# Performance work log

Hardware: AMD Instinct MI355X
Metric: run time of the kernel (lower is better)

Reference implementation:

```python
import jax, jax.numpy as jnp
import numpy as np

B, N, C, K = 2, 8192, 128, 16

def _mlp2(h, W1, b1, W2, b2):
    return jax.nn.relu(h @ W1 + b1) @ W2 + b2

def setup_inputs() -> dict:
    key = jax.random.key(0)
    ks = jax.random.split(key, 20)
    s = lambda d: 1.0 / np.sqrt(d)
    inp = {
        "x": jax.random.normal(ks[0], (B, N, C), jnp.float32),
        "position": jax.random.normal(ks[1], (B, N, 3), jnp.float32),
        "Wq": jax.random.normal(ks[2], (C, C), jnp.float32) * s(C),
        "bq": jnp.zeros((C,), jnp.float32),
        "Wk": jax.random.normal(ks[3], (C, C), jnp.float32) * s(C),
        "bk": jnp.zeros((C,), jnp.float32),
        "Wv": jax.random.normal(ks[4], (C, C), jnp.float32) * s(C),
        "bv": jnp.zeros((C,), jnp.float32),
        "Wp1": jax.random.normal(ks[5], (3, C), jnp.float32) * s(3),
        "bp1": jnp.zeros((C,), jnp.float32),
        "Wp2": jax.random.normal(ks[6], (C, C), jnp.float32) * s(C),
        "bp2": jnp.zeros((C,), jnp.float32),
        "Wg1": jax.random.normal(ks[7], (C, C), jnp.float32) * s(C),
        "bg1": jnp.zeros((C,), jnp.float32),
        "Wg2": jax.random.normal(ks[8], (C, C), jnp.float32) * s(C),
        "bg2": jnp.zeros((C,), jnp.float32),
    }
    return inp

def reference(x, position, Wq, bq, Wk, bk, Wv, bv, Wp1, bp1, Wp2, bp2, Wg1, bg1, Wg2, bg2):
    # kNN via squared pairwise distances (monotone in cdist, same topk indices)
    p2 = jnp.sum(position * position, axis=-1)                       # (B,N)
    d2 = p2[:, :, None] + p2[:, None, :] - 2.0 * jnp.einsum("bnd,bmd->bnm", position, position)
    _, idx = jax.lax.top_k(-d2, K)                                    # (B,N,K) nearest (incl self)

    gather = jax.vmap(lambda arr, i: arr[i])                          # per-batch fancy gather
    neighbors = gather(x, idx)                                        # (B,N,K,C)
    pos_nb = gather(position, idx)                                    # (B,N,K,3)

    q = x @ Wq + bq                                                   # (B,N,C)
    k = neighbors @ Wk + bk                                           # (B,N,K,C)
    v = neighbors @ Wv + bv                                           # (B,N,K,C)

    # positional MLP only at gathered pairs (same math as all-pairs-then-gather)
    rel = position[:, :, None, :] - pos_nb                            # (B,N,K,3)
    pe = _mlp2(rel, Wp1, bp1, Wp2, bp2)                               # (B,N,K,C)

    scale = 1.0 / jnp.sqrt(jnp.float32(C))
    attn = (q[:, :, None, :] - k + pe) * scale
    attn = _mlp2(attn, Wg1, bg1, Wg2, bg2)
    attn = jax.nn.softmax(attn, axis=2)                               # softmax over K neighbors
    out = jnp.sum(attn * (v + pe), axis=2)                            # (B,N,C)
    return out
```

## Files before the change

### kernel.cpp

```cpp
#include <hip/hip_runtime.h>
#include <hip/hip_bf16.h>
#include <stdint.h>

#define NPTS 8192
#define CDIM 128
#define KNNK 16
#define WELEMF 16384
#define SCALE 0.08838834764831845f
#define FLDS_BYTES 78848
#define GRES 16
#define NCELL (GRES*GRES*GRES)

typedef __attribute__((ext_vector_type(4))) float f32x4;
typedef __attribute__((ext_vector_type(8))) short s16x8;

__device__ __forceinline__ unsigned short to_bf16(float f){
  union { __hip_bfloat16 h; unsigned short u; } v;
  v.h = __float2bfloat16(f);
  return v.u;
}

__device__ __forceinline__ s16x8 cvt8(const float* p){
  float4 lo = *(const float4*)p;
  float4 hi = *(const float4*)(p + 4);
  s16x8 f;
  f[0]=(short)to_bf16(lo.x); f[1]=(short)to_bf16(lo.y);
  f[2]=(short)to_bf16(lo.z); f[3]=(short)to_bf16(lo.w);
  f[4]=(short)to_bf16(hi.x); f[5]=(short)to_bf16(hi.y);
  f[6]=(short)to_bf16(hi.z); f[7]=(short)to_bf16(hi.w);
  return f;
}

__device__ __forceinline__ unsigned mapf_u(unsigned s){
  return s ^ (0x80000000u | (unsigned)(((int)s) >> 31));
}
__device__ __forceinline__ float unmapf_u(unsigned u){
  unsigned r = (u & 0x80000000u) ? (u ^ 0x80000000u) : ~u;
  return __uint_as_float(r);
}

__global__ __launch_bounds__(256) void zero_init_kernel(int* __restrict__ counts,
                                                        unsigned* __restrict__ bbox)
{
  int t = blockIdx.x*256 + threadIdx.x;
  if (t < 2*NCELL) counts[t] = 0;
  if (t < 12) bbox[t] = ((t % 6) < 3) ? 0xFFFFFFFFu : 0u;
}

__global__ __launch_bounds__(256) void prep_kernel(
    const float* __restrict__ Wq, const float* __restrict__ Wk,
    const float* __restrict__ Wv, const float* __restrict__ Wp2,
    const float* __restrict__ Wg1, const float* __restrict__ Wg2,
    const float* __restrict__ pos,
    unsigned short* __restrict__ wt, float4* __restrict__ pos4,
    unsigned* __restrict__ bbox)
{
  int t = blockIdx.x*256 + threadIdx.x;
  if (t < 6*WELEMF){
    int w = t >> 14, f = t & (WELEMF-1);
    int i = f & 7, ln = (f >> 3) & 63, kkct = f >> 9;
    int kk = kkct & 3, ct = kkct >> 2;
    int kdim = kk*32 + (ln >> 4)*8 + i, col = ct*16 + (ln & 15);
    const float* src = (w==0)?Wq:(w==1)?Wk:(w==2)?Wv:(w==3)?Wp2:(w==4)?Wg1:Wg2;
    float v = src[kdim*CDIM + col];
    if (w == 1) v = -v;
    wt[t] = to_bf16(v);
  } else {
    int m = t - 6*WELEMF;
    float xx = pos[m*3+0], yy = pos[m*3+1], zz = pos[m*3+2];
    float p2 = __fadd_rn(__fadd_rn(__fmul_rn(xx,xx), __fmul_rn(yy,yy)), __fmul_rn(zz,zz));
    pos4[m] = make_float4(xx, yy, zz, p2);
    unsigned mnx = mapf_u(__float_as_uint(xx)), mny = mapf_u(__float_as_uint(yy)), mnz = mapf_u(__float_as_uint(zz));
    unsigned mxx = mnx, mxy = mny, mxz = mnz;
#pragma unroll
    for (int off = 1; off < 64; off <<= 1){
      mnx = min(mnx, (unsigned)__shfl_xor((int)mnx, off));
      mny = min(mny, (unsigned)__shfl_xor((int)mny, off));
      mnz = min(mnz, (unsigned)__shfl_xor((int)mnz, off));
      mxx = max(mxx, (unsigned)__shfl_xor((int)mxx, off));
      mxy = max(mxy, (unsigned)__shfl_xor((int)mxy, off));
      mxz = max(mxz, (unsigned)__shfl_xor((int)mxz, off));
    }
    if ((threadIdx.x & 63) == 0){
      int b = m >> 13;
      atomicMin(&bbox[b*6+0], mnx); atomicMin(&bbox[b*6+1], mny); atomicMin(&bbox[b*6+2], mnz);
      atomicMax(&bbox[b*6+3], mxx); atomicMax(&bbox[b*6+4], mxy); atomicMax(&bbox[b*6+5], mxz);
    }
  }
}

__global__ __launch_bounds__(256) void bin_count_kernel(
    const float4* __restrict__ pos4, const unsigned* __restrict__ bbox,
    int* __restrict__ counts, int* __restrict__ cellId)
{
  int m = blockIdx.x*256 + threadIdx.x;
  int b = m >> 13;
  float4 p = pos4[m];
  float lox = unmapf_u(bbox[b*6+0]), loy = unmapf_u(bbox[b*6+1]), loz = unmapf_u(bbox[b*6+2]);
  float hix = unmapf_u(bbox[b*6+3]), hiy = unmapf_u(bbox[b*6+4]), hiz = unmapf_u(bbox[b*6+5]);
  int ix = min(GRES-1, max(0, (int)((p.x - lox) * ((float)GRES/(hix-lox)))));
  int iy = min(GRES-1, max(0, (int)((p.y - loy) * ((float)GRES/(hiy-loy)))));
  int iz = min(GRES-1, max(0, (int)((p.z - loz) * ((float)GRES/(hiz-loz)))));
  int cid = (iz*GRES + iy)*GRES + ix;
  cellId[m] = cid;
  atomicAdd(&counts[b*NCELL + cid], 1);
}

__global__ __launch_bounds__(1024) void scan_kernel(
    const int* __restrict__ counts, int* __restrict__ starts, int* __restrict__ cursor)
{
  __shared__ int part[1024];
  int b = blockIdx.x, t = threadIdx.x;
  const int* c = counts + b*NCELL;
  int* s = starts + b*(NCELL+1);
  int* cur = cursor + b*NCELL;
  int base = t*4, sum = 0;
  for (int i = 0; i < 4; ++i) sum += c[base+i];
  part[t] = sum; __syncthreads();
  for (int off = 1; off < 1024; off <<= 1){
    int v = (t >= off) ? part[t-off] : 0;
    __syncthreads();
    part[t] += v;
    __syncthreads();
  }
  int run = (t > 0) ? part[t-1] : 0;
  for (int i = 0; i < 4; ++i){ int cc = c[base+i]; s[base+i] = run; cur[base+i] = run; run += cc; }
  if (t == 1023) s[NCELL] = run;
}

__global__ __launch_bounds__(256) void scatter_kernel(
    const float4* __restrict__ pos4, const int* __restrict__ cellId,
    int* __restrict__ cursor, float4* __restrict__ spos4)
{
  int m = blockIdx.x*256 + threadIdx.x;
  int b = m >> 13;
  float4 p = pos4[m];
  int dst = atomicAdd(&cursor[b*NCELL + cellId[m]], 1);
  spos4[(b<<13) + dst] = make_float4(p.x, p.y, p.z, __uint_as_float((unsigned)(m & (NPTS-1))));
}

__global__ __launch_bounds__(256) void knn_grid_kernel(
    const float4* __restrict__ spos4, const int* __restrict__ starts,
    const unsigned* __restrict__ bbox, int* __restrict__ idxout)
{
  const int tid = threadIdx.x, lane = tid & 63;
  const int sub = lane >> 4, sl = lane & 15, gbase = sub*16;
  const int w = tid >> 6;
  const int g = blockIdx.x*16 + w*4 + sub;
  const int b = g >> 13, n = g & (NPTS-1);
  const float4* sp = spos4 + ((size_t)b<<13);
  const int*    st = starts + b*(NCELL+1);

  const float4 q4 = sp[n];
  const int orig = __float_as_int(q4.w);
  const float qx = q4.x, qy = q4.y, qz = q4.z;
  const float q2 = __fadd_rn(__fadd_rn(__fmul_rn(qx,qx), __fmul_rn(qy,qy)), __fmul_rn(qz,qz));

  float lox = unmapf_u(bbox[b*6+0]), loy = unmapf_u(bbox[b*6+1]), loz = unmapf_u(bbox[b*6+2]);
  float hix = unmapf_u(bbox[b*6+3]), hiy = unmapf_u(bbox[b*6+4]), hiz = unmapf_u(bbox[b*6+5]);
  float cwx = (hix-lox)*(1.0f/GRES), cwy = (hiy-loy)*(1.0f/GRES), cwz = (hiz-loz)*(1.0f/GRES);
  int cx = min(GRES-1, max(0, (int)((qx - lox) * ((float)GRES/(hix-lox)))));
  int cy = min(GRES-1, max(0, (int)((qy - loy) * ((float)GRES/(hiy-loy)))));
  int cz = min(GRES-1, max(0, (int)((qz - loz) * ((float)GRES/(hiz-loz)))));

  unsigned khi = 0xFFFFFFFFu, klo = 0xFFFFFFFFu;
  float Tf = __builtin_inff();

  auto insert = [&](unsigned ihi, unsigned ilo){
    unsigned phi = (unsigned)__builtin_amdgcn_update_dpp(0, (int)khi, 0x111, 0xF, 0xF, false);
    unsigned plo = (unsigned)__builtin_amdgcn_update_dpp(0, (int)klo, 0x111, 0xF, 0xF, false);
    bool gt  = (khi > ihi) || (khi == ihi && klo > ilo);
    bool pgt = (sl != 0) && ((phi > ihi) || (phi == ihi && plo > ilo));
    khi = gt ? (pgt ? phi : ihi) : khi;
    klo = gt ? (pgt ? plo : ilo) : klo;
  };
  auto updT = [&](){
    unsigned t15 = (unsigned)__shfl((int)khi, gbase + 15);
    Tf = (t15 >= 0xFF800000u) ? __builtin_inff() : unmapf_u(t15);
  };

  bool gdone = false;
  for (int R = 1; R <= GRES-1; ++R){
    const bool first = (R == 1);
    const int per = 8*R, w1 = 2*R-1;
    const int ntask = first ? 9 : (per + 2*w1*w1);
    for (int tb = 0; tb < ntask; tb += 16){
      int t = tb + sl;
      int dy = 0, dz = 0, gx0 = 0, gx1 = -1;
      bool valid = (!gdone) && (t < ntask);
      if (first){
        if (valid){ dy = t % 3 - 1; dz = t / 3 - 1; }
        gx0 = max(cx-1, 0); gx1 = min(cx+1, GRES-1);
      } else if (valid){
        if (t < per){
          int s2 = 2*(2*R+1);
          if (t < s2){ dz = (t < 2*R+1) ? -R : R; dy = t % (2*R+1) - R; }
          else { int u = t - s2; dy = (u & 1) ? R : -R; dz = (u >> 1) - (R-1); }
          gx0 = max(cx-R, 0); gx1 = min(cx+R, GRES-1);
        } else {
          int i = t - per, ri = i >> 1;
          dy = ri % w1 - (R-1); dz = ri / w1 - (R-1);
          int gx = cx + ((i & 1) ? R : -R);
          gx0 = gx; gx1 = gx;
          valid = gx >= 0 && gx <= GRES-1;
        }
      }
      int gy = cy + dy, gz = cz + dz;
      valid = valid && gy >= 0 && gy < GRES && gz >= 0 && gz < GRES && gx0 <= gx1;
      int s0 = 0, s1 = 0;
      if (valid){ int cb = (gz*GRES + gy)*GRES; s0 = st[cb + gx0]; s1 = st[cb + gx1 + 1]; }
      unsigned long long bal = __ballot(valid && (s1 > s0));
      unsigned cm = (unsigned)((bal >> gbase) & 0xFFFFull);
      while (__any(cm != 0)){
        bool act = (cm != 0);
        int srow = act ? __builtin_ctz(cm) : 0;
        if (act) cm &= cm - 1;
        int cs = __shfl(s0, gbase + srow);
        int ce = __shfl(s1, gbase + srow);
        if (!act){ cs = 0; ce = 0; }
        for (int p0 = cs; p0 < ce; p0 += 16){
          int mm = p0 + sl;
          bool v = mm < ce;
          float4 c = v ? sp[mm] : make_float4(0.f,0.f,0.f,0.f);
          float c2  = __fadd_rn(__fadd_rn(__fmul_rn(c.x,c.x), __fmul_rn(c.y,c.y)), __fmul_rn(c.z,c.z));
          float dot = __builtin_fmaf(c.z, qz, __builtin_fmaf(c.y, qy, __fmul_rn(c.x, qx)));
          float d2  = __fsub_rn(__fadd_rn(q2, c2), __fadd_rn(dot, dot));
          int oi = __float_as_int(c.w);
          bool ins = v && (d2 <= Tf);
          unsigned long long ib = __ballot(ins);
          unsigned im = (unsigned)((ib >> gbase) & 0xFFFFull);
          if (__any(im != 0)){
            while (__any(im != 0)){
              bool a2 = (im != 0);
              int s = a2 ? __builtin_ctz(im) : 0;
              if (a2) im &= im - 1;
              unsigned dvb = (unsigned)__shfl((int)__float_as_uint(d2), gbase + s);
              int ov = __shfl(oi, gbase + s);
              if (a2) insert(mapf_u(dvb), (unsigned)ov);
            }
            updT();
          }
        }
      }
    }
    const float big = 1e30f;
    float dxlo = (cx-R <= 0)      ? big : (qx - (lox + (float)(cx-R)*cwx));
    float dxhi = (cx+R >= GRES-1) ? big : ((lox + (float)(cx+R+1)*cwx) - qx);
    float dylo = (cy-R <= 0)      ? big : (qy - (loy + (float)(cy-R)*cwy));
    float dyhi = (cy+R >= GRES-1) ? big : ((loy + (float)(cy+R+1)*cwy) - qy);
    float dzlo = (cz-R <= 0)      ? big : (qz - (loz + (float)(cz-R)*cwz));
    float dzhi = (cz+R >= GRES-1) ? big : ((loz + (float)(cz+R+1)*cwz) - qz);
    float dmin = fminf(fminf(fminf(dxlo,dxhi), fminf(dylo,dyhi)), fminf(dzlo,dzhi));
    bool full = dmin >= 1e29f;
    dmin = fmaxf(dmin, 0.0f);
    float dmin2 = dmin*dmin;
    bool stop = full || (Tf + 1e-4f + Tf*1e-5f < dmin2);
    gdone = gdone || stop;
    if (__all(gdone)) break;
  }
  idxout[(((size_t)b<<13) + orig)*KNNK + sl] = (int)klo;
}

__global__ __launch_bounds__(512, 2) void fused_kernel(
    const float* __restrict__ x, const float* __restrict__ pos,
    const float* __restrict__ bq, const float* __restrict__ bk,
    const float* __restrict__ bv, const float* __restrict__ Wp1,
    const float* __restrict__ bp1, const float* __restrict__ bp2,
    const float* __restrict__ bg1, const float* __restrict__ bg2,
    const int* __restrict__ idxws, const unsigned short* __restrict__ wt,
    float* __restrict__ out)
{
  extern __shared__ char smem[];
  char* Sbase = smem;
  char* Tbase = smem + 32768;
  float* blds = (float*)(smem + 65536);
  float* q_lds = (float*)(smem + 70656);

  const int tid = threadIdx.x;
  const int lane = tid & 63, w = tid >> 6;
  const int r = lane & 15, grp = lane >> 4;
  const int pbase = blockIdx.x * 16;
  const int b = pbase >> 13;

  auto gll = [&](int s, char* dst){
#pragma unroll
    for (int k = 0; k < 4; ++k){
      int c = w*4 + k;
      unsigned short* g = const_cast<unsigned short*>(wt) + (size_t)s*WELEMF + c*512 + lane*8;
      __builtin_amdgcn_global_load_lds(
        (const __attribute__((address_space(1))) void*)g,
        (__attribute__((address_space(3))) void*)(dst + c*1024), 16, 0, 0);
    }
  };
  auto ldS = [&](int ct, int kk) -> s16x8 {
    return *(const s16x8*)&((unsigned short*)Sbase)[((ct*4 + kk)*64 + lane)*8];
  };
  auto ldT = [&](int ct, int kk) -> s16x8 {
    return *(const s16x8*)&((unsigned short*)Tbase)[((ct*4 + kk)*64 + lane)*8];
  };

  gll(0, Sbase);
  gll(3, Tbase);

  for (int e = tid; e < 1280; e += 512){
    float v;
    if      (e < 128)  v = bq[e];
    else if (e < 256)  v = bk[e-128];
    else if (e < 384)  v = bv[e-256];
    else if (e < 512)  v = bp2[e-384];
    else if (e < 640)  v = bg1[e-512];
    else if (e < 768)  v = bg2[e-640];
    else if (e < 896)  v = bp1[e-768];
    else               v = Wp1[e-896];
    blds[e] = v;
  }
  int nbr[2]; float relx[2], rely[2], relz[2];
#pragma unroll
  for (int j = 0; j < 2; ++j){
    int gp = pbase + w*2 + j;
    nbr[j] = idxws[(size_t)gp*KNNK + r];
    const float* pq = pos + (size_t)gp*3;
    const float* pn = pos + ((size_t)b*NPTS + nbr[j])*3;
    relx[j] = pq[0]-pn[0]; rely[j] = pq[1]-pn[1]; relz[j] = pq[2]-pn[2];
  }
  s16x8 qa[4];
  {
    const float* xr = x + (size_t)(pbase + r)*CDIM;
#pragma unroll
    for (int kk = 0; kk < 4; ++kk) qa[kk] = cvt8(xr + kk*32 + grp*8);
  }
  __syncthreads();

  {
    f32x4 qacc = (f32x4){0.f,0.f,0.f,0.f};
#pragma unroll
    for (int kk = 0; kk < 4; ++kk)
      qacc = __builtin_amdgcn_mfma_f32_16x16x32_bf16(qa[kk], ldS(w,kk), qacc, 0,0,0);
    int col = w*16 + r;
#pragma unroll
    for (int jj = 0; jj < 4; ++jj){
      int row = grp*4 + jj;
      q_lds[row*CDIM + col] = qacc[jj] + blds[col];
    }
  }
  s16x8 pf[2][4];
#pragma unroll
  for (int j = 0; j < 2; ++j)
#pragma unroll
    for (int kk = 0; kk < 4; ++kk){
      s16x8 f;
#pragma unroll
      for (int i = 0; i < 8; ++i){
        int kc = kk*32 + grp*8 + i;
        float s = relx[j]*blds[896+kc] + rely[j]*blds[1024+kc] + relz[j]*blds[1152+kc] + blds[768+kc];
        f[i] = (short)to_bf16(fmaxf(s, 0.f));
      }
      pf[j][kk] = f;
    }
  __syncthreads();
  gll(1, Sbase);

  f32x4 at[2][8], av[2][8];
#pragma unroll
  for (int j=0;j<2;++j)
#pragma unroll
    for (int ct=0;ct<8;++ct) at[j][ct] = (f32x4){0.f,0.f,0.f,0.f};
#pragma unroll
  for (int ct=0;ct<8;++ct)
#pragma unroll
    for (int kk=0;kk<4;++kk){
      s16x8 bw = ldT(ct,kk);
#pragma unroll
      for (int j=0;j<2;++j)
        at[j][ct] = __builtin_amdgcn_mfma_f32_16x16x32_bf16(pf[j][kk], bw, at[j][ct], 0,0,0);
    }
  s16x8 nf[2][4];
#pragma unroll
  for (int j=0;j<2;++j)
#pragma unroll
    for (int kk=0;kk<4;++kk)
      nf[j][kk] = cvt8(x + ((size_t)b*NPTS + nbr[j])*CDIM + kk*32 + grp*8);

  __syncthreads();
  gll(2, Tbase);
#pragma unroll
  for (int j=0;j<2;++j)
#pragma unroll
    for (int ct=0;ct<8;++ct) av[j][ct] = at[j][ct];
#pragma unroll
  for (int ct=0;ct<8;++ct)
#pragma unroll
    for (int kk=0;kk<4;++kk){
      s16x8 bw = ldS(ct,kk);
#pragma unroll
      for (int j=0;j<2;++j) at[j][ct] = __builtin_amdgcn_mfma_f32_16x16x32_bf16(nf[j][kk], bw, at[j][ct], 0,0,0);
    }
  __syncthreads();
  gll(4, Sbase);
#pragma unroll
  for (int ct=0;ct<8;++ct)
#pragma unroll
    for (int kk=0;kk<4;++kk){
      s16x8 bw = ldT(ct,kk);
#pragma unroll
      for (int j=0;j<2;++j) av[j][ct] = __builtin_amdgcn_mfma_f32_16x16x32_bf16(nf[j][kk], bw, av[j][ct], 0,0,0);
    }
#pragma unroll
  for (int j=0;j<2;++j){
    int prow = (w*2+j)*CDIM;
#pragma unroll
    for (int ct=0;ct<8;++ct){
      int col = ct*16+r;
      float add = q_lds[prow+col] + blds[384+col] - blds[128+col];
#pragma unroll
      for (int jj=0;jj<4;++jj) at[j][ct][jj] = (at[j][ct][jj] + add)*SCALE;
    }
  }
  __syncthreads();

  unsigned short* tj = (unsigned short*)Tbase + w*2048;
  s16x8 tf[2][4];
#pragma unroll
  for (int j=0;j<2;++j){
#pragma unroll
    for (int ct=0;ct<8;++ct){
      int base = (ct>>1)*512 + ((ct&1)*2 + (r>>3))*128 + (r&7);
#pragma unroll
      for (int jj=0;jj<4;++jj)
        tj[base + (grp*4+jj)*8] = to_bf16(at[j][ct][jj]);
    }
#pragma unroll
    for (int kk=0;kk<4;++kk)
      tf[j][kk] = *(const s16x8*)&tj[(kk*64 + lane)*8];
  }
  f32x4 hacc[2][8];
#pragma unroll
  for (int j=0;j<2;++j)
#pragma unroll
    for (int ct=0;ct<8;++ct) hacc[j][ct] = (f32x4){0.f,0.f,0.f,0.f};
#pragma unroll
  for (int ct=0;ct<8;++ct)
#pragma unroll
    for (int kk=0;kk<4;++kk){
      s16x8 bw = ldS(ct,kk);
#pragma unroll
      for (int j=0;j<2;++j)
        hacc[j][ct] = __builtin_amdgcn_mfma_f32_16x16x32_bf16(tf[j][kk], bw, hacc[j][ct], 0,0,0);
    }
  __syncthreads();
  gll(5, Sbase);
  s16x8 hf[2][4];
#pragma unroll
  for (int j=0;j<2;++j){
#pragma unroll
    for (int ct=0;ct<8;++ct){
      int base = (ct>>1)*512 + ((ct&1)*2 + (r>>3))*128 + (r&7);
      int col = ct*16+r; float bb = blds[512+col];
#pragma unroll
      for (int jj=0;jj<4;++jj)
        tj[base + (grp*4+jj)*8] = to_bf16(fmaxf(hacc[j][ct][jj]+bb, 0.f));
    }
#pragma unroll
    for (int kk=0;kk<4;++kk)
      hf[j][kk] = *(const s16x8*)&tj[(kk*64 + lane)*8];
  }
  __syncthreads();
  f32x4 gacc[2][8];
#pragma unroll
  for (int j=0;j<2;++j)
#pragma unroll
    for (int ct=0;ct<8;++ct) gacc[j][ct] = (f32x4){0.f,0.f,0.f,0.f};
#pragma unroll
  for (int ct=0;ct<8;++ct)
#pragma unroll
    for (int kk=0;kk<4;++kk){
      s16x8 bw = ldS(ct,kk);
#pragma unroll
      for (int j=0;j<2;++j)
        gacc[j][ct] = __builtin_amdgcn_mfma_f32_16x16x32_bf16(hf[j][kk], bw, gacc[j][ct], 0,0,0);
    }
#pragma unroll
  for (int j=0;j<2;++j){
#pragma unroll
    for (int ct=0;ct<8;++ct){
      int col = ct*16+r;
      float gb = blds[640+col];
      float g0v = gacc[j][ct][0]+gb, g1v = gacc[j][ct][1]+gb;
      float g2v = gacc[j][ct][2]+gb, g3v = gacc[j][ct][3]+gb;
      float mx = fmaxf(fmaxf(g0v,g1v), fmaxf(g2v,g3v));
      mx = fmaxf(mx, __shfl_xor(mx,16));
      mx = fmaxf(mx, __shfl_xor(mx,32));
      float e0=__expf(g0v-mx), e1=__expf(g1v-mx), e2=__expf(g2v-mx), e3=__expf(g3v-mx);
      float vb = blds[256+col] + blds[384+col];
      float ss = e0+e1+e2+e3;
      float oo = e0*(av[j][ct][0]+vb) + e1*(av[j][ct][1]+vb)
               + e2*(av[j][ct][2]+vb) + e3*(av[j][ct][3]+vb);
      ss += __shfl_xor(ss,16); ss += __shfl_xor(ss,32);
      oo += __shfl_xor(oo,16); oo += __shfl_xor(oo,32);
      if (grp == 0) out[(size_t)(pbase + w*2 + j)*CDIM + col] = oo/ss;
    }
  }
}

extern "C" void kernel_launch(void* const* d_in, const int* in_sizes, int n_in,
                              void* d_out, int out_size, void* d_ws, size_t ws_size,
                              hipStream_t stream)
{
  const float* x    = (const float*)d_in[0];
  const float* pos  = (const float*)d_in[1];
  const float* Wq   = (const float*)d_in[2];
  const float* bq   = (const float*)d_in[3];
  const float* Wk   = (const float*)d_in[4];
  const float* bk   = (const float*)d_in[5];
  const float* Wv   = (const float*)d_in[6];
  const float* bv   = (const float*)d_in[7];
  const float* Wp1  = (const float*)d_in[8];
  const float* bp1  = (const float*)d_in[9];
  const float* Wp2  = (const float*)d_in[10];
  const float* bp2  = (const float*)d_in[11];
  const float* Wg1  = (const float*)d_in[12];
  const float* bg1  = (const float*)d_in[13];
  const float* Wg2  = (const float*)d_in[14];
  const float* bg2  = (const float*)d_in[15];
  float* out = (float*)d_out;

  char* ws = (char*)d_ws;
  int*            idxs   = (int*)ws;
  unsigned short* wt     = (unsigned short*)(ws + 1048576);
  float4*         pos4   = (float4*)(ws + 1257472);
  float4*         spos4  = (float4*)(ws + 1519616);
  int*            cellId = (int*)(ws + 1847296);
  int*            counts = (int*)(ws + 1912832);
  int*            starts = (int*)(ws + 2174976);
  int*            cursor = (int*)(ws + 2437376);
  unsigned*       bbox   = (unsigned*)(ws + 2699520);

  hipFuncSetAttribute((const void*)fused_kernel,
                      hipFuncAttributeMaxDynamicSharedMemorySize, FLDS_BYTES);

  zero_init_kernel<<<32, 256, 0, stream>>>(counts, bbox);
  prep_kernel<<<448, 256, 0, stream>>>(Wq, Wk, Wv, Wp2, Wg1, Wg2, pos, wt, pos4, bbox);
  bin_count_kernel<<<64, 256, 0, stream>>>(pos4, bbox, counts, cellId);
  scan_kernel<<<2, 1024, 0, stream>>>(counts, starts, cursor);
  scatter_kernel<<<64, 256, 0, stream>>>(pos4, cellId, cursor, spos4);
  knn_grid_kernel<<<1024, 256, 0, stream>>>(spos4, starts, bbox, idxs);
  fused_kernel<<<1024, 512, FLDS_BYTES, stream>>>(x, pos, bq, bk, bv, Wp1, bp1, bp2,
                                                  bg1, bg2, idxs, wt, out);
}
```

Before: 211.2 us.

## Stage neighborhood candidate points and cell starts into LDS for kNN grid search

Each block cooperatively loads the cell-start table and the sorted candidate points for a 7x5x5 cell box around a representative query cell into shared memory, assigning per-row offsets up to a fixed capacity. The kNN candidate loop then reads from LDS when a cell row is staged and falls back to global memory otherwise. This aims to cut repeated global/L2 loads of the same candidate points across the 16 queries in a block, at the cost of about 40KB of LDS (reducing occupancy), extra syncs, and a serial prefix loop on one thread.

```diff
diff --git a/kernel.cpp b/kernel.cpp
--- a/kernel.cpp
+++ b/kernel.cpp
@@ -10,6 +10,8 @@
 #define FLDS_BYTES 78848
 #define GRES 16
 #define NCELL (GRES*GRES*GRES)
+#define KCAP 2560
+#define UNSTAGED 0x40000000
 
 typedef __attribute__((ext_vector_type(4))) float f32x4;
 typedef __attribute__((ext_vector_type(8))) short s16x8;
@@ -143,6 +145,11 @@
     const float4* __restrict__ spos4, const int* __restrict__ starts,
     const unsigned* __restrict__ bbox, int* __restrict__ idxout)
 {
+  __shared__ float4 ptsLds[KCAP];
+  __shared__ int    stLds[25*8];
+  __shared__ int    rowBase[25];
+  __shared__ int    mcell[4];
+
   const int tid = threadIdx.x, lane = tid & 63;
   const int sub = lane >> 4, sl = lane & 15, gbase = sub*16;
   const int w = tid >> 6;
@@ -162,6 +169,36 @@
   int cx = min(GRES-1, max(0, (int)((qx - lox) * ((float)GRES/(hix-lox)))));
   int cy = min(GRES-1, max(0, (int)((qy - loy) * ((float)GRES/(hiy-loy)))));
   int cz = min(GRES-1, max(0, (int)((qz - loz) * ((float)GRES/(hiz-loz)))));
+
+  if (tid == 128){ mcell[0] = cx; mcell[1] = cy; mcell[2] = cz; }
+  __syncthreads();
+  const int bx0 = max(mcell[0]-3, 0), bx1 = min(mcell[0]+3, GRES-1);
+  const int by0 = max(mcell[1]-2, 0), by1 = min(mcell[1]+2, GRES-1);
+  const int bz0 = max(mcell[2]-2, 0), bz1 = min(mcell[2]+2, GRES-1);
+  const int xe = bx1-bx0+1, ye = by1-by0+1, ze = bz1-bz0+1;
+  const int nrows = ye*ze;
+  for (int e = tid; e < nrows*(xe+1); e += 256){
+    int ri = e/(xe+1), xi = e - ri*(xe+1);
+    int gy = by0 + ri % ye, gz = bz0 + ri / ye;
+    stLds[ri*8 + xi] = st[(gz*GRES + gy)*GRES + bx0 + xi];
+  }
+  __syncthreads();
+  if (tid == 0){
+    int cum = 0;
+    for (int ri = 0; ri < nrows; ++ri){
+      int g0 = stLds[ri*8], len = stLds[ri*8+xe] - g0;
+      if (cum + len <= KCAP){ rowBase[ri] = cum - g0; cum += len; }
+      else rowBase[ri] = UNSTAGED;
+    }
+  }
+  __syncthreads();
+  for (int ri = 0; ri < nrows; ++ri){
+    int rb = rowBase[ri];
+    if (rb == UNSTAGED) continue;
+    int g0 = stLds[ri*8], g1 = stLds[ri*8+xe];
+    for (int i = g0 + tid; i < g1; i += 256) ptsLds[rb + i] = sp[i];
+  }
+  __syncthreads();
 
   unsigned khi = 0xFFFFFFFFu, klo = 0xFFFFFFFFu;
   float Tf = __builtin_inff();
@@ -207,8 +244,19 @@
       }
       int gy = cy + dy, gz = cz + dz;
       valid = valid && gy >= 0 && gy < GRES && gz >= 0 && gz < GRES && gx0 <= gx1;
-      int s0 = 0, s1 = 0;
-      if (valid){ int cb = (gz*GRES + gy)*GRES; s0 = st[cb + gx0]; s1 = st[cb + gx1 + 1]; }
+      int s0 = 0, s1 = 0, lbase = UNSTAGED;
+      if (valid){
+        bool inbox = gy >= by0 && gy <= by1 && gz >= bz0 && gz <= bz1
+                  && gx0 >= bx0 && gx1 <= bx1;
+        if (inbox){
+          int ri = (gz-bz0)*ye + (gy-by0);
+          s0 = stLds[ri*8 + (gx0-bx0)];
+          s1 = stLds[ri*8 + (gx1-bx0+1)];
+          lbase = rowBase[ri];
+        } else {
+          int cb = (gz*GRES + gy)*GRES; s0 = st[cb + gx0]; s1 = st[cb + gx1 + 1];
+        }
+      }
       unsigned long long bal = __ballot(valid && (s1 > s0));
       unsigned cm = (unsigned)((bal >> gbase) & 0xFFFFull);
       while (__any(cm != 0)){
@@ -217,11 +265,14 @@
         if (act) cm &= cm - 1;
         int cs = __shfl(s0, gbase + srow);
         int ce = __shfl(s1, gbase + srow);
+        int lb = __shfl(lbase, gbase + srow);
         if (!act){ cs = 0; ce = 0; }
         for (int p0 = cs; p0 < ce; p0 += 16){
           int mm = p0 + sl;
           bool v = mm < ce;
-          float4 c = v ? sp[mm] : make_float4(0.f,0.f,0.f,0.f);
+          float4 c;
+          if (v) c = (lb != UNSTAGED) ? ptsLds[lb + mm] : sp[mm];
+          else   c = make_float4(0.f,0.f,0.f,0.f);
           float c2  = __fadd_rn(__fadd_rn(__fmul_rn(c.x,c.x), __fmul_rn(c.y,c.y)), __fmul_rn(c.z,c.z));
           float dot = __builtin_fmaf(c.z, qz, __builtin_fmaf(c.y, qy, __fmul_rn(c.x, qx)));
           float d2  = __fsub_rn(__fadd_rn(q2, c2), __fadd_rn(dot, dot));
```

Result: slower. 248.5 us (+17.7%).

## Fuse grid-build stages into one kernel and pre-convert x to bf16

Applied to the files above, without the earlier changes.

Replaces the separate zero-init, bbox, bin-count, scan and scatter kernels with one per-batch kernel that does counting, scanning and scattering in shared memory. This removes four launches and the global atomics on counts and cursor. prep_kernel now also converts x to a bf16 copy in the workspace, so the fused kernel can load bf16 neighbor rows directly and skip converting them from fp32 on every gather. The bf16 path is used only when the workspace is large enough and falls back to the old path otherwise. The grid build now runs on just 2 blocks, which limits its parallelism.

```diff
diff --git a/kernel.cpp b/kernel.cpp
--- a/kernel.cpp
+++ b/kernel.cpp
@@ -39,24 +39,97 @@
   return __uint_as_float(r);
 }
 
-__global__ __launch_bounds__(256) void zero_init_kernel(int* __restrict__ counts,
-                                                        unsigned* __restrict__ bbox)
+__global__ __launch_bounds__(1024) void gridbuild_kernel(
+    const float* __restrict__ pos, float4* __restrict__ spos4,
+    int* __restrict__ starts, unsigned* __restrict__ bboxg)
 {
-  int t = blockIdx.x*256 + threadIdx.x;
-  if (t < 2*NCELL) counts[t] = 0;
-  if (t < 12) bbox[t] = ((t % 6) < 3) ? 0xFFFFFFFFu : 0u;
+  __shared__ int cnt[NCELL];
+  __shared__ int part[1024];
+  __shared__ unsigned bbl[6];
+  const int b = blockIdx.x, t = threadIdx.x;
+  for (int i = t; i < NCELL; i += 1024) cnt[i] = 0;
+  if (t < 3) bbl[t] = 0xFFFFFFFFu;
+  else if (t < 6) bbl[t] = 0u;
+  __syncthreads();
+
+  float4 p[8];
+  unsigned mn0=~0u, mn1=~0u, mn2=~0u, mx0=0u, mx1=0u, mx2=0u;
+#pragma unroll
+  for (int i = 0; i < 8; ++i){
+    int m = t + i*1024;
+    const float* pp = pos + ((size_t)b*NPTS + m)*3;
+    float xx = pp[0], yy = pp[1], zz = pp[2];
+    float p2 = __fadd_rn(__fadd_rn(__fmul_rn(xx,xx), __fmul_rn(yy,yy)), __fmul_rn(zz,zz));
+    p[i] = make_float4(xx, yy, zz, p2);
+    unsigned ux = mapf_u(__float_as_uint(xx));
+    unsigned uy = mapf_u(__float_as_uint(yy));
+    unsigned uz = mapf_u(__float_as_uint(zz));
+    mn0 = min(mn0, ux); mn1 = min(mn1, uy); mn2 = min(mn2, uz);
+    mx0 = max(mx0, ux); mx1 = max(mx1, uy); mx2 = max(mx2, uz);
+  }
+#pragma unroll
+  for (int off = 1; off < 64; off <<= 1){
+    mn0 = min(mn0, (unsigned)__shfl_xor((int)mn0, off));
+    mn1 = min(mn1, (unsigned)__shfl_xor((int)mn1, off));
+    mn2 = min(mn2, (unsigned)__shfl_xor((int)mn2, off));
+    mx0 = max(mx0, (unsigned)__shfl_xor((int)mx0, off));
+    mx1 = max(mx1, (unsigned)__shfl_xor((int)mx1, off));
+    mx2 = max(mx2, (unsigned)__shfl_xor((int)mx2, off));
+  }
+  if ((t & 63) == 0){
+    atomicMin(&bbl[0], mn0); atomicMin(&bbl[1], mn1); atomicMin(&bbl[2], mn2);
+    atomicMax(&bbl[3], mx0); atomicMax(&bbl[4], mx1); atomicMax(&bbl[5], mx2);
+  }
+  __syncthreads();
+  const float lox = unmapf_u(bbl[0]), loy = unmapf_u(bbl[1]), loz = unmapf_u(bbl[2]);
+  const float hix = unmapf_u(bbl[3]), hiy = unmapf_u(bbl[4]), hiz = unmapf_u(bbl[5]);
+
+  int cid[8];
+#pragma unroll
+  for (int i = 0; i < 8; ++i){
+    int ix = min(GRES-1, max(0, (int)((p[i].x - lox) * ((float)GRES/(hix-lox)))));
+    int iy = min(GRES-1, max(0, (int)((p[i].y - loy) * ((float)GRES/(hiy-loy)))));
+    int iz = min(GRES-1, max(0, (int)((p[i].z - loz) * ((float)GRES/(hiz-loz)))));
+    cid[i] = (iz*GRES + iy)*GRES + ix;
+    atomicAdd(&cnt[cid[i]], 1);
+  }
+  __syncthreads();
+  const int base = t*4;
+  int c0 = cnt[base], c1 = cnt[base+1], c2 = cnt[base+2], c3 = cnt[base+3];
+  part[t] = c0+c1+c2+c3;
+  __syncthreads();
+  for (int off = 1; off < 1024; off <<= 1){
+    int v = (t >= off) ? part[t-off] : 0;
+    __syncthreads();
+    part[t] += v;
+    __syncthreads();
+  }
+  int run = (t > 0) ? part[t-1] : 0;
+  int* stb = starts + b*(NCELL+1);
+  int r1 = run + c0, r2 = r1 + c1, r3 = r2 + c2;
+  stb[base] = run; stb[base+1] = r1; stb[base+2] = r2; stb[base+3] = r3;
+  if (t == 1023) stb[NCELL] = r3 + c3;
+  cnt[base] = run; cnt[base+1] = r1; cnt[base+2] = r2; cnt[base+3] = r3;
+  __syncthreads();
+  float4* spb = spos4 + ((size_t)b << 13);
+#pragma unroll
+  for (int i = 0; i < 8; ++i){
+    int m = t + i*1024;
+    int dst = atomicAdd(&cnt[cid[i]], 1);
+    spb[dst] = make_float4(p[i].x, p[i].y, p[i].z, __uint_as_float((unsigned)m));
+  }
+  if (t < 6) bboxg[b*6 + t] = bbl[t];
 }
 
 __global__ __launch_bounds__(256) void prep_kernel(
     const float* __restrict__ Wq, const float* __restrict__ Wk,
     const float* __restrict__ Wv, const float* __restrict__ Wp2,
     const float* __restrict__ Wg1, const float* __restrict__ Wg2,
-    const float* __restrict__ pos,
-    unsigned short* __restrict__ wt, float4* __restrict__ pos4,
-    unsigned* __restrict__ bbox)
+    const float* __restrict__ x,
+    unsigned short* __restrict__ wt, unsigned short* __restrict__ xbf)
 {
-  int t = blockIdx.x*256 + threadIdx.x;
-  if (t < 6*WELEMF){
+  if (blockIdx.x < 384){
+    int t = blockIdx.x*256 + threadIdx.x;
     int w = t >> 14, f = t & (WELEMF-1);
     int i = f & 7, ln = (f >> 3) & 63, kkct = f >> 9;
     int kk = kkct & 3, ct = kkct >> 2;
@@ -66,77 +139,10 @@
     if (w == 1) v = -v;
     wt[t] = to_bf16(v);
   } else {
-    int m = t - 6*WELEMF;
-    float xx = pos[m*3+0], yy = pos[m*3+1], zz = pos[m*3+2];
-    float p2 = __fadd_rn(__fadd_rn(__fmul_rn(xx,xx), __fmul_rn(yy,yy)), __fmul_rn(zz,zz));
-    pos4[m] = make_float4(xx, yy, zz, p2);
-    unsigned mnx = mapf_u(__float_as_uint(xx)), mny = mapf_u(__float_as_uint(yy)), mnz = mapf_u(__float_as_uint(zz));
-    unsigned mxx = mnx, mxy = mny, mxz = mnz;
-#pragma unroll
-    for (int off = 1; off < 64; off <<= 1){
-      mnx = min(mnx, (unsigned)__shfl_xor((int)mnx, off));
-      mny = min(mny, (unsigned)__shfl_xor((int)mny, off));
-      mnz = min(mnz, (unsigned)__shfl_xor((int)mnz, off));
-      mxx = max(mxx, (unsigned)__shfl_xor((int)mxx, off));
-      mxy = max(mxy, (unsigned)__shfl_xor((int)mxy, off));
-      mxz = max(mxz, (unsigned)__shfl_xor((int)mxz, off));
-    }
-    if ((threadIdx.x & 63) == 0){
-      int b = m >> 13;
-      atomicMin(&bbox[b*6+0], mnx); atomicMin(&bbox[b*6+1], mny); atomicMin(&bbox[b*6+2], mnz);
-      atomicMax(&bbox[b*6+3], mxx); atomicMax(&bbox[b*6+4], mxy); atomicMax(&bbox[b*6+5], mxz);
-    }
-  }
-}
-
-__global__ __launch_bounds__(256) void bin_count_kernel(
-    const float4* __restrict__ pos4, const unsigned* __restrict__ bbox,
-    int* __restrict__ counts, int* __restrict__ cellId)
-{
-  int m = blockIdx.x*256 + threadIdx.x;
-  int b = m >> 13;
-  float4 p = pos4[m];
-  float lox = unmapf_u(bbox[b*6+0]), loy = unmapf_u(bbox[b*6+1]), loz = unmapf_u(bbox[b*6+2]);
-  float hix = unmapf_u(bbox[b*6+3]), hiy = unmapf_u(bbox[b*6+4]), hiz = unmapf_u(bbox[b*6+5]);
-  int ix = min(GRES-1, max(0, (int)((p.x - lox) * ((float)GRES/(hix-lox)))));
-  int iy = min(GRES-1, max(0, (int)((p.y - loy) * ((float)GRES/(hiy-loy)))));
-  int iz = min(GRES-1, max(0, (int)((p.z - loz) * ((float)GRES/(hiz-loz)))));
-  int cid = (iz*GRES + iy)*GRES + ix;
-  cellId[m] = cid;
-  atomicAdd(&counts[b*NCELL + cid], 1);
-}
-
-__global__ __launch_bounds__(1024) void scan_kernel(
-    const int* __restrict__ counts, int* __restrict__ starts, int* __restrict__ cursor)
-{
-  __shared__ int part[1024];
-  int b = blockIdx.x, t = threadIdx.x;
-  const int* c = counts + b*NCELL;
-  int* s = starts + b*(NCELL+1);
-  int* cur = cursor + b*NCELL;
-  int base = t*4, sum = 0;
-  for (int i = 0; i < 4; ++i) sum += c[base+i];
-  part[t] = sum; __syncthreads();
-  for (int off = 1; off < 1024; off <<= 1){
-    int v = (t >= off) ? part[t-off] : 0;
-    __syncthreads();
-    part[t] += v;
-    __syncthreads();
-  }
-  int run = (t > 0) ? part[t-1] : 0;
-  for (int i = 0; i < 4; ++i){ int cc = c[base+i]; s[base+i] = run; cur[base+i] = run; run += cc; }
-  if (t == 1023) s[NCELL] = run;
-}
-
-__global__ __launch_bounds__(256) void scatter_kernel(
-    const float4* __restrict__ pos4, const int* __restrict__ cellId,
-    int* __restrict__ cursor, float4* __restrict__ spos4)
-{
-  int m = blockIdx.x*256 + threadIdx.x;
-  int b = m >> 13;
-  float4 p = pos4[m];
-  int dst = atomicAdd(&cursor[b*NCELL + cellId[m]], 1);
-  spos4[(b<<13) + dst] = make_float4(p.x, p.y, p.z, __uint_as_float((unsigned)(m & (NPTS-1))));
+    size_t e = ((size_t)(blockIdx.x - 384)*256 + threadIdx.x) * 8;
+    s16x8 v = cvt8(x + e);
+    *(s16x8*)&xbf[e] = v;
+  }
 }
 
 __global__ __launch_bounds__(256) void knn_grid_kernel(
@@ -268,6 +274,7 @@
     const float* __restrict__ bp1, const float* __restrict__ bp2,
     const float* __restrict__ bg1, const float* __restrict__ bg2,
     const int* __restrict__ idxws, const unsigned short* __restrict__ wt,
+    const unsigned short* __restrict__ xbf,
     float* __restrict__ out)
 {
   extern __shared__ char smem[];
@@ -324,7 +331,11 @@
     relx[j] = pq[0]-pn[0]; rely[j] = pq[1]-pn[1]; relz[j] = pq[2]-pn[2];
   }
   s16x8 qa[4];
-  {
+  if (xbf){
+    const unsigned short* xr = xbf + (size_t)(pbase + r)*CDIM;
+#pragma unroll
+    for (int kk = 0; kk < 4; ++kk) qa[kk] = *(const s16x8*)&xr[kk*32 + grp*8];
+  } else {
     const float* xr = x + (size_t)(pbase + r)*CDIM;
 #pragma unroll
     for (int kk = 0; kk < 4; ++kk) qa[kk] = cvt8(xr + kk*32 + grp*8);
@@ -375,11 +386,21 @@
         at[j][ct] = __builtin_amdgcn_mfma_f32_16x16x32_bf16(pf[j][kk], bw, at[j][ct], 0,0,0);
     }
   s16x8 nf[2][4];
-#pragma unroll
-  for (int j=0;j<2;++j)
-#pragma unroll
-    for (int kk=0;kk<4;++kk)
-      nf[j][kk] = cvt8(x + ((size_t)b*NPTS + nbr[j])*CDIM + kk*32 + grp*8);
+  if (xbf){
+#pragma unroll
+    for (int j=0;j<2;++j){
+      const unsigned short* xr = xbf + ((size_t)b*NPTS + nbr[j])*CDIM;
+#pragma unroll
+      for (int kk=0;kk<4;++kk)
+        nf[j][kk] = *(const s16x8*)&xr[kk*32 + grp*8];
+    }
+  } else {
+#pragma unroll
+    for (int j=0;j<2;++j)
+#pragma unroll
+      for (int kk=0;kk<4;++kk)
+        nf[j][kk] = cvt8(x + ((size_t)b*NPTS + nbr[j])*CDIM + kk*32 + grp*8);
+  }
 
   __syncthreads();
   gll(2, Tbase);
@@ -527,23 +548,19 @@
   char* ws = (char*)d_ws;
   int*            idxs   = (int*)ws;
   unsigned short* wt     = (unsigned short*)(ws + 1048576);
-  float4*         pos4   = (float4*)(ws + 1257472);
   float4*         spos4  = (float4*)(ws + 1519616);
-  int*            cellId = (int*)(ws + 1847296);
-  int*            counts = (int*)(ws + 1912832);
   int*            starts = (int*)(ws + 2174976);
-  int*            cursor = (int*)(ws + 2437376);
   unsigned*       bbox   = (unsigned*)(ws + 2699520);
+  const size_t XBF_OFF = 2699776;
+  const size_t XBF_SZ  = (size_t)2*NPTS*CDIM*2;
+  unsigned short* xbf = (ws_size >= XBF_OFF + XBF_SZ) ? (unsigned short*)(ws + XBF_OFF) : nullptr;
 
   hipFuncSetAttribute((const void*)fused_kernel,
                       hipFuncAttributeMaxDynamicSharedMemorySize, FLDS_BYTES);
 
-  zero_init_kernel<<<32, 256, 0, stream>>>(counts, bbox);
-  prep_kernel<<<448, 256, 0, stream>>>(Wq, Wk, Wv, Wp2, Wg1, Wg2, pos, wt, pos4, bbox);
-  bin_count_kernel<<<64, 256, 0, stream>>>(pos4, bbox, counts, cellId);
-  scan_kernel<<<2, 1024, 0, stream>>>(counts, starts, cursor);
-  scatter_kernel<<<64, 256, 0, stream>>>(pos4, cellId, cursor, spos4);
+  gridbuild_kernel<<<2, 1024, 0, stream>>>(pos, spos4, starts, bbox);
+  prep_kernel<<<xbf ? 1408 : 384, 256, 0, stream>>>(Wq, Wk, Wv, Wp2, Wg1, Wg2, x, wt, xbf);
   knn_grid_kernel<<<1024, 256, 0, stream>>>(spos4, starts, bbox, idxs);
   fused_kernel<<<1024, 512, FLDS_BYTES, stream>>>(x, pos, bq, bk, bv, Wp1, bp1, bp2,
-                                                  bg1, bg2, idxs, wt, out);
-}
+                                                  bg1, bg2, idxs, wt, xbf, out);
+}
```

Result: faster. 186.6 us (-11.7%).
